# Performance work log

Measured on AMD Instinct MI355X. Metric: run time of the kernel, lower is better.

The kernel has to match this reference:

```python
import jax, jax.numpy as jnp
import numpy as np
from jax import lax

B, C, L = 64, 768, 197
DEG = 3          # KACN Chebyshev degree
KW = 3           # conv kernel size
EPS = 1e-5       # BatchNorm eps
END_X = 14.0     # RoPE grid width (14x14 patch grid + 1 CLS token)


def _conv1d(x, W):
    # x: (B, Cin, L), W: (Cout, Cin, K); padding=1 keeps length
    return lax.conv_general_dilated(x, W, window_strides=(1,), padding=[(1, 1)],
                                    dimension_numbers=('NCH', 'OIH', 'NCH'))


def _batchnorm(y, scale, bias):
    # training-mode BatchNorm1d: biased stats over (batch, length)
    mean = jnp.mean(y, axis=(0, 2), keepdims=True)
    var = jnp.var(y, axis=(0, 2), keepdims=True)
    return (y - mean) * lax.rsqrt(var + EPS) * scale[None, :, None] + bias[None, :, None]


def _kacn_proj(x, W, scale, bias):
    # KACNConv1DLayer (groups=1): cos(arange(deg+1) * arccos(tanh(x))) basis, conv, BN
    b, c, l = x.shape
    z = jnp.arccos(jnp.tanh(x))[:, :, None, :] * jnp.arange(DEG + 1, dtype=x.dtype)[None, None, :, None]
    z = jnp.cos(z).reshape(b, c * (DEG + 1), l)  # (B, C*(DEG+1), L), channel-major pairing
    return _batchnorm(_conv1d(z, W), scale, bias)


def _rope(t, cosang, sinang):
    # rotate consecutive channel pairs; t: (B, N, C), cos/sin: (N, C//2)
    b, n, c = t.shape
    p = t.reshape(b, n, c // 2, 2)
    a, bb = p[..., 0], p[..., 1]
    ra = a * cosang[None] - bb * sinang[None]
    rb = a * sinang[None] + bb * cosang[None]
    return jnp.stack([ra, rb], axis=-1).reshape(b, n, c)


def reference(x, Wq, Wk, Wv, bnq_s, bnq_b, bnk_s, bnk_b, bnv_s, bnv_b, gamma, freqs, norm_s, norm_b):
    q = _kacn_proj(x, Wq, bnq_s, bnq_b)
    k = _kacn_proj(x, Wk, bnk_s, bnk_b)
    v = _kacn_proj(x, Wv, bnv_s, bnv_b)
    b, c, l = v.shape
    Q = q.transpose(0, 2, 1)  # (B, L, C)
    K = k.transpose(0, 2, 1)
    # mixed 2D RoPE angles (num_heads=1): t_x, t_y over 14x14 grid
    t = jnp.arange(l - 1, dtype=x.dtype)
    tx = jnp.mod(t, END_X)
    ty = jnp.floor(t / END_X)
    ang = tx[:, None] * freqs[0][None, :] + ty[:, None] * freqs[1][None, :]  # (L-1, C//2)
    cosang, sinang = jnp.cos(ang), jnp.sin(ang)
    # token 0 (CLS) is not rotated
    Qr = jnp.concatenate([Q[:, :1], _rope(Q[:, 1:], cosang, sinang)], axis=1)
    Kr = jnp.concatenate([K[:, :1], _rope(K[:, 1:], cosang, sinang)], axis=1)
    energy = jnp.einsum('bic,bjc->bij', Qr, Kr)          # unscaled, as in the module
    att = jax.nn.softmax(energy, axis=-1)
    out = jnp.einsum('bcj,bij->bci', v, att)             # v @ att^T
    return _batchnorm(gamma[0] * x + out, norm_s, norm_b)


def setup_inputs() -> dict:
    key = jax.random.key(0)
    ks = jax.random.split(key, 5)
    std = 1.0 / (C * (DEG + 1) * KW)
    x = jax.random.normal(ks[0], (B, C, L), dtype=jnp.float32)
    Wq = jax.random.normal(ks[1], (C, C * (DEG + 1), KW), dtype=jnp.float32) * std
    Wk = jax.random.normal(ks[2], (C, C * (DEG + 1), KW), dtype=jnp.float32) * std
    Wv = jax.random.normal(ks[3], (C, C * (DEG + 1), KW), dtype=jnp.float32) * std
    ones = jnp.ones((C,), jnp.float32)
    zeros = jnp.zeros((C,), jnp.float32)
    # init_2d_freqs(dim=C, num_heads=1, theta=10, rotate=True).view(2, -1)
    mag = 1.0 / 10.0 ** (np.arange(0, C, 4)[: C // 4].astype(np.float32) / C)
    ang = float(jax.random.uniform(ks[4], ())) * 2.0 * np.pi
    fx = np.concatenate([mag * np.cos(ang), mag * np.cos(np.pi / 2 + ang)])
    fy = np.concatenate([mag * np.sin(ang), mag * np.sin(np.pi / 2 + ang)])
    freqs = jnp.asarray(np.stack([fx, fy], axis=0), dtype=jnp.float32)  # (2, C//2)
    return {"x": x, "Wq": Wq, "Wk": Wk, "Wv": Wv,
            "bnq_s": ones, "bnq_b": zeros, "bnk_s": ones, "bnk_b": zeros,
            "bnv_s": ones, "bnv_b": zeros,
            "gamma": jnp.zeros((1,), jnp.float32), "freqs": freqs,
            "norm_s": ones, "norm_b": zeros}
```

## Files before the change

kernel.cpp:

```cpp
#include <hip/hip_runtime.h>

#define CCH 768
#define LL  197
#define L199 199
#define KC  2304
#define KTOT 6912
#define MK2 1769472
#define NVALID 12736
#define NROW 12608

typedef __bf16 bf16x8 __attribute__((ext_vector_type(8)));
typedef float f32x4 __attribute__((ext_vector_type(4)));
typedef float f32x16 __attribute__((ext_vector_type(16)));

__device__ __forceinline__ unsigned short f2bf(float f) {
  unsigned int u = __float_as_uint(f);
  u += 0x7FFFu + ((u >> 16) & 1u);
  return (unsigned short)(u >> 16);
}
__device__ __forceinline__ float bf2f(unsigned short h) {
  return __uint_as_float(((unsigned int)h) << 16);
}

__global__ void bias_k(const float* __restrict__ Wq, const float* __restrict__ Wk,
                       const float* __restrict__ Wv, float* __restrict__ bias3) {
  int u = blockIdx.x * 256 + threadIdx.x;
  if (u >= 9 * 768) return;
  int proj = u / 2304, rem = u % 2304, tap = rem / 768, m = rem % 768;
  const float* W = proj == 0 ? Wq : (proj == 1 ? Wk : Wv);
  float s = 0.f;
  for (int c = 0; c < 768; ++c) s += W[((size_t)m * 3072 + c * 4) * 3 + tap];
  bias3[u] = s;
}

__global__ void pack_w3(const float* __restrict__ Wq, const float* __restrict__ Wk,
                        const float* __restrict__ Wv, unsigned short* __restrict__ Apack,
                        size_t pack1_halves) {
  int u = blockIdx.x * 256 + threadIdx.x;
  if (u >= MK2) return;
  int proj = blockIdx.y;
  const float* W = proj == 0 ? Wq : (proj == 1 ? Wk : Wv);
  unsigned short* Ahi = Apack + (size_t)proj * pack1_halves;
  unsigned short* Alo = Ahi + (size_t)768 * KTOT;
  int m = u / KC, kc = u % KC;
  int c = kc / 3, dm1 = kc % 3;
  int ci = c * 4 + dm1 + 1;
  const float* src = W + ((size_t)m * 3072 + ci) * 3;
#pragma unroll
  for (int tap = 0; tap < 3; ++tap) {
    float f = src[tap];
    unsigned short hi = f2bf(f);
    unsigned short lo = f2bf(f - bf2f(hi));
    size_t idx = (size_t)m * KTOT + tap * KC + kc;
    Ahi[idx] = hi;
    Alo[idx] = lo;
  }
}

__global__ void z_kernel(const float* __restrict__ x, unsigned short* __restrict__ Zhi,
                         unsigned short* __restrict__ Zlo) {
  __shared__ float zs[3][32][33];
  int c0 = blockIdx.x * 32, l0 = blockIdx.y * 32, b = blockIdx.z;
  int t = threadIdx.x;
#pragma unroll
  for (int s = 0; s < 4; ++s) {
    int u = t + 256 * s;
    int rc = u >> 5, cl = u & 31;
    float v = 0.f;
    if (l0 + cl < LL) v = x[((size_t)b * CCH + c0 + rc) * LL + l0 + cl];
    float t1 = tanhf(v);
    zs[0][rc][cl] = t1;
    zs[1][rc][cl] = 2.f * t1 * t1 - 1.f;
    zs[2][rc][cl] = t1 * (4.f * t1 * t1 - 3.f);
  }
  __syncthreads();
#pragma unroll
  for (int s = 0; s < 12; ++s) {
    int w = t + 256 * s;
    int rl = w / 96, cc = w % 96;
    if (l0 + rl < LL) {
      int cl2 = cc / 3, dm1 = cc % 3;
      float v = zs[dm1][cl2][rl];
      unsigned short hi = f2bf(v);
      unsigned short lo = f2bf(v - bf2f(hi));
      size_t row = (size_t)b * L199 + 1 + l0 + rl;
      Zhi[row * KC + c0 * 3 + cc] = hi;
      Zlo[row * KC + c0 * 3 + cc] = lo;
    }
  }
}

__global__ void zero_zpad(unsigned short* __restrict__ Zhi, unsigned short* __restrict__ Zlo) {
  int u = blockIdx.x * 256 + threadIdx.x;
  if (u >= 132 * KC) return;
  int rowi = u / KC, c = u % KC;
  size_t r = (rowi < 128) ? ((size_t)(rowi >> 1) * L199 + (size_t)(rowi & 1) * 198)
                          : ((size_t)NVALID + rowi - 128);
  Zhi[r * KC + c] = 0;
  Zlo[r * KC + c] = 0;
}

#define GLL(SRC, DST) \
  __builtin_amdgcn_global_load_lds( \
      (const __attribute__((address_space(1))) void*)(SRC), \
      (__attribute__((address_space(3))) void*)(DST), 16, 0, 0)

__global__ __launch_bounds__(512, 2) void conv_gemm3(const unsigned short* __restrict__ Apack,
                                                     const unsigned short* __restrict__ Zhi,
                                                     const unsigned short* __restrict__ Zlo,
                                                     const float* __restrict__ bias3,
                                                     float* __restrict__ Oqk,
                                                     float* __restrict__ Ov) {
  __shared__ unsigned short lds[2 * 4 * 8192];
  const int bid = blockIdx.x;
  const int xcd = bid & 7, loc = bid >> 3;
  const int wg = (xcd < 2) ? (xcd * 57 + loc) : (114 + (xcd - 2) * 56 + loc);
  const int n_t = wg / 9, rem = wg % 9;
  const int proj = rem / 3, m_t = rem % 3;
  const int m_blk = m_t * 256, n_blk = n_t * 256;
  const unsigned short* Ahi = Apack + (size_t)proj * 2 * 768 * KTOT;
  const unsigned short* Alo = Ahi + (size_t)768 * KTOT;
  const float* bias3p = bias3 + proj * 2304;
  float* Op = (proj == 2) ? Ov : Oqk + (size_t)proj * NROW * CCH;

  const int t = threadIdx.x;
  const int wave = t >> 6, lane = t & 63;
  const int wm = (wave >> 2) * 128, wn = (wave & 3) * 64;
  f32x16 acc[4][2] = {};

  const int lt = ((lane >> 4) & 1) * 512 + (lane >> 5) * 128 + (lane & 15) * 8;
  const int auoff = (wm >> 4) * 512 + lt;
  const int buoff = (wn >> 4) * 512 + lt;

  const int prow = lane & 15;
  const int kch = lane >> 4;
  const unsigned short* srcs[8];
  int doff[8];
#pragma unroll
  for (int j = 0; j < 8; ++j) {
    int u = (wave << 3) + j;
    int tile = u >> 4, p = u & 15;
    doff[j] = tile * 8192 + p * 512;
    int r;
    const unsigned short* g;
    int rs;
    if (tile < 2) {
      r = m_blk + p * 16 + prow;
      g = (tile == 0) ? Ahi : Alo;
      rs = KTOT;
    } else {
      r = n_blk + p * 16 + prow;
      if (r > 12737) r = 12737;
      g = (tile == 2) ? Zhi : Zlo;
      rs = KC;
    }
    srcs[j] = g + (size_t)r * rs + kch * 8;
  }

#pragma unroll
  for (int j = 0; j < 8; ++j) GLL(srcs[j], lds + doff[j]);
#pragma unroll
  for (int j = 0; j < 8; ++j) GLL(srcs[j] + 32, lds + 32768 + doff[j]);
#pragma unroll
  for (int j = 0; j < 8; ++j) srcs[j] += 64;

#define STEP32(LB)                                                                \
  {                                                                               \
    _Pragma("unroll") for (int ks = 0; ks < 2; ++ks) {                            \
      bf16x8 ah[4], al[4], bh[2], bl[2];                                          \
      _Pragma("unroll") for (int mb = 0; mb < 4; ++mb) {                          \
        ah[mb] = *(const bf16x8*)((LB) + auoff + mb * 1024 + ks * 256);           \
        al[mb] = *(const bf16x8*)((LB) + 8192 + auoff + mb * 1024 + ks * 256);    \
      }                                                                           \
      _Pragma("unroll") for (int nb = 0; nb < 2; ++nb) {                          \
        bh[nb] = *(const bf16x8*)((LB) + 16384 + buoff + nb * 1024 + ks * 256);   \
        bl[nb] = *(const bf16x8*)((LB) + 24576 + buoff + nb * 1024 + ks * 256);   \
      }                                                                           \
      __builtin_amdgcn_s_setprio(1);                                              \
      _Pragma("unroll") for (int mb = 0; mb < 4; ++mb)                            \
      _Pragma("unroll") for (int nb = 0; nb < 2; ++nb) {                          \
        acc[mb][nb] = __builtin_amdgcn_mfma_f32_32x32x16_bf16(ah[mb], bh[nb], acc[mb][nb], 0, 0, 0); \
        acc[mb][nb] = __builtin_amdgcn_mfma_f32_32x32x16_bf16(ah[mb], bl[nb], acc[mb][nb], 0, 0, 0); \
        acc[mb][nb] = __builtin_amdgcn_mfma_f32_32x32x16_bf16(al[mb], bh[nb], acc[mb][nb], 0, 0, 0); \
      }                                                                           \
      __builtin_amdgcn_s_setprio(0);                                              \
    }                                                                             \
  }

  const int NIT = KTOT / 32;
  for (int i = 0; i < NIT - 1; ++i) {
    asm volatile("s_waitcnt vmcnt(8)\n\ts_barrier" ::: "memory");
    __builtin_amdgcn_sched_barrier(0);
    const unsigned short* lb = lds + ((i & 1) ? 32768 : 0);
    STEP32(lb);
    asm volatile("s_waitcnt lgkmcnt(0)\n\ts_barrier" ::: "memory");
    __builtin_amdgcn_sched_barrier(0);
    if (i < NIT - 2) {
      unsigned short* ld = lds + ((i & 1) ? 32768 : 0);
#pragma unroll
      for (int j = 0; j < 8; ++j) {
        GLL(srcs[j], ld + doff[j]);
        srcs[j] += 32;
      }
    }
  }
  asm volatile("s_waitcnt vmcnt(0)\n\ts_barrier" ::: "memory");
  __builtin_amdgcn_sched_barrier(0);
  STEP32(lds + 32768);

  int rowarr[2];
  bool val[2], v0[2], v2[2];
#pragma unroll
  for (int nb = 0; nb < 2; ++nb) {
    int n = n_blk + wn + nb * 32 + (lane & 31);
    int b = n / L199, nl = n - b * L199;
    val[nb] = (n < NVALID) && (nl < LL);
    rowarr[nb] = b * LL + nl;
    v0[nb] = (nl == 0);
    v2[nb] = (nl == 196);
  }
#pragma unroll
  for (int mb = 0; mb < 4; ++mb) {
#pragma unroll
    for (int q = 0; q < 4; ++q) {
      int m = m_blk + wm + mb * 32 + q * 8 + (lane >> 5) * 4;
      f32x4 b0 = *(const f32x4*)(bias3p + m);
      f32x4 b1 = *(const f32x4*)(bias3p + 768 + m);
      f32x4 b2 = *(const f32x4*)(bias3p + 1536 + m);
      f32x4 bs = b0 + b1 + b2;
#pragma unroll
      for (int nb = 0; nb < 2; ++nb) {
        if (val[nb]) {
          f32x4 r;
          r[0] = acc[mb][nb][q * 4 + 0];
          r[1] = acc[mb][nb][q * 4 + 1];
          r[2] = acc[mb][nb][q * 4 + 2];
          r[3] = acc[mb][nb][q * 4 + 3];
          r += bs;
          if (v0[nb]) r -= b0;
          if (v2[nb]) r -= b2;
          *(f32x4*)(Op + (size_t)rowarr[nb] * CCH + m) = r;
        }
      }
    }
  }
#undef STEP32
}

__global__ void zero_f32(float* __restrict__ p, int n) {
  int u = blockIdx.x * 256 + threadIdx.x;
  if (u < n) p[u] = 0.f;
}

__global__ void bn_stats(const float* __restrict__ Oqk, const float* __restrict__ Ov,
                         float* __restrict__ Ssum, float* __restrict__ Ssq) {
  int proj = blockIdx.z;
  int cb = blockIdx.x * 64;
  int rb = blockIdx.y;
  int t = threadIdx.x;
  int ch = cb + (t & 63);
  int phase = t >> 6;
  const float* Op = (proj == 2) ? Ov : Oqk + (size_t)proj * NROW * CCH;
  float s = 0.f, q = 0.f;
  for (int r = rb * 394 + phase; r < rb * 394 + 394; r += 4) {
    float v = Op[(size_t)r * CCH + ch];
    s += v; q += v * v;
  }
  __shared__ float rs[256], rq[256];
  rs[t] = s; rq[t] = q;
  __syncthreads();
  if (t < 64) {
    float S = rs[t] + rs[t + 64] + rs[t + 128] + rs[t + 192];
    float Q = rq[t] + rq[t + 64] + rq[t + 128] + rq[t + 192];
    atomicAdd(&Ssum[proj * CCH + cb + t], S);
    atomicAdd(&Ssq[proj * CCH + cb + t], Q);
  }
}

__global__ void bn_fin(const float* __restrict__ Ssum, const float* __restrict__ Ssq,
                       const float* __restrict__ sq, const float* __restrict__ bq,
                       const float* __restrict__ sk, const float* __restrict__ bk,
                       const float* __restrict__ sv, const float* __restrict__ bv,
                       float* __restrict__ abn) {
  int u = blockIdx.x * 256 + threadIdx.x;
  if (u >= 3 * CCH) return;
  int proj = u / CCH, ch = u % CCH;
  float mean = Ssum[u] / 12608.f;
  float var = Ssq[u] / 12608.f - mean * mean;
  const float* sc = proj == 0 ? sq : (proj == 1 ? sk : sv);
  const float* bi = proj == 0 ? bq : (proj == 1 ? bk : bv);
  float a = sc[ch] * rsqrtf(var + 1e-5f);
  abn[u * 2] = a;
  abn[u * 2 + 1] = bi[ch] - mean * a;
}

__global__ void rope_pack(const float* __restrict__ Oqk, const float* __restrict__ abn,
                          const float* __restrict__ freqs, float* __restrict__ Qr,
                          float* __restrict__ Kr) {
  size_t u = (size_t)blockIdx.x * 256 + threadIdx.x;
  if (u >= 64ull * LL * 384) return;
  int c2 = (int)(u % 384);
  int l = (int)((u / 384) % LL);
  int b = (int)(u / (384ull * LL));
  size_t rowO = ((size_t)b * LL + l) * CCH + 2 * c2;
  const float* Ok = Oqk + (size_t)NROW * CCH;
  float q0 = Oqk[rowO], q1 = Oqk[rowO + 1];
  float k0 = Ok[rowO], k1 = Ok[rowO + 1];
  float aq0 = abn[(2 * c2) * 2],                bq0 = abn[(2 * c2) * 2 + 1];
  float aq1 = abn[(2 * c2 + 1) * 2],            bq1 = abn[(2 * c2 + 1) * 2 + 1];
  float ak0 = abn[(CCH + 2 * c2) * 2],          bk0 = abn[(CCH + 2 * c2) * 2 + 1];
  float ak1 = abn[(CCH + 2 * c2 + 1) * 2],      bk1 = abn[(CCH + 2 * c2 + 1) * 2 + 1];
  q0 = q0 * aq0 + bq0; q1 = q1 * aq1 + bq1;
  k0 = k0 * ak0 + bk0; k1 = k1 * ak1 + bk1;
  if (l > 0) {
    int tt = l - 1;
    float tx = (float)(tt % 14), ty = (float)(tt / 14);
    float ang = tx * freqs[c2] + ty * freqs[384 + c2];
    float sn, cs;
    sincosf(ang, &sn, &cs);
    float r0 = q0 * cs - q1 * sn, r1 = q0 * sn + q1 * cs;
    q0 = r0; q1 = r1;
    r0 = k0 * cs - k1 * sn; r1 = k0 * sn + k1 * cs;
    k0 = r0; k1 = r1;
  }
  size_t rowT = ((size_t)b * LL + l) * CCH + 2 * c2;
  Qr[rowT] = q0; Qr[rowT + 1] = q1;
  Kr[rowT] = k0; Kr[rowT + 1] = k1;
}

__global__ void energy_k(const float* __restrict__ Qr, const float* __restrict__ Kr,
                         float* __restrict__ E) {
  __shared__ float Qs[32][33], Ks[32][33];
  int i0 = blockIdx.x * 32, j0 = blockIdx.y * 32, b = blockIdx.z;
  int t = threadIdx.x, tj = t & 31, ti = t >> 5;
  float acc[4] = {0.f, 0.f, 0.f, 0.f};
  const float* Qb = Qr + (size_t)b * LL * CCH;
  const float* Kb = Kr + (size_t)b * LL * CCH;
  for (int k0 = 0; k0 < CCH; k0 += 32) {
    __syncthreads();
#pragma unroll
    for (int s = 0; s < 4; ++s) {
      int u = t + 256 * s, r = u >> 5, cc = u & 31;
      Qs[r][cc] = (i0 + r < LL) ? Qb[(size_t)(i0 + r) * CCH + k0 + cc] : 0.f;
      Ks[r][cc] = (j0 + r < LL) ? Kb[(size_t)(j0 + r) * CCH + k0 + cc] : 0.f;
    }
    __syncthreads();
#pragma unroll
    for (int kk = 0; kk < 32; ++kk) {
      float kv = Ks[tj][kk];
#pragma unroll
      for (int q = 0; q < 4; ++q) acc[q] += Qs[ti * 4 + q][kk] * kv;
    }
  }
#pragma unroll
  for (int q = 0; q < 4; ++q) {
    int i = i0 + ti * 4 + q, j = j0 + tj;
    if (i < LL && j < LL) E[((size_t)b * LL + i) * LL + j] = acc[q];
  }
}

__global__ void softmax_k(float* __restrict__ E) {
  int row = blockIdx.x;
  int lane = threadIdx.x;
  float* Er = E + (size_t)row * LL;
  float v[4];
  float m = -3.4e38f;
#pragma unroll
  for (int q = 0; q < 4; ++q) {
    int j = lane + 64 * q;
    v[q] = (j < LL) ? Er[j] : -3.4e38f;
    m = fmaxf(m, v[q]);
  }
  for (int off = 32; off; off >>= 1) m = fmaxf(m, __shfl_down(m, off));
  m = __shfl(m, 0);
  float s = 0.f;
#pragma unroll
  for (int q = 0; q < 4; ++q) {
    int j = lane + 64 * q;
    v[q] = (j < LL) ? expf(v[q] - m) : 0.f;
    s += v[q];
  }
  for (int off = 32; off; off >>= 1) s += __shfl_down(s, off);
  s = __shfl(s, 0);
  float inv = 1.f / s;
#pragma unroll
  for (int q = 0; q < 4; ++q) {
    int j = lane + 64 * q;
    if (j < LL) Er[j] = v[q] * inv;
  }
}

__global__ void av_k(const float* __restrict__ att, const float* __restrict__ Ov,
                     const float* __restrict__ abn, float* __restrict__ OA) {
  __shared__ float As[32][33];
  __shared__ float Vs[32][64];
  int i0 = blockIdx.x * 32, c0 = blockIdx.y * 64, b = blockIdx.z;
  int t = threadIdx.x, tc = t & 63, tq = t >> 6;
  const float* attb = att + (size_t)b * LL * LL;
  float acc[8] = {};
  for (int j0 = 0; j0 < LL; j0 += 32) {
    __syncthreads();
#pragma unroll
    for (int s = 0; s < 4; ++s) {
      int u = t + 256 * s, r = u >> 5, cc = u & 31;
      As[r][cc] = (i0 + r < LL && j0 + cc < LL) ? attb[(size_t)(i0 + r) * LL + j0 + cc] : 0.f;
    }
#pragma unroll
    for (int s = 0; s < 8; ++s) {
      int u = t + 256 * s, r = u >> 6, cc = u & 63;
      Vs[r][cc] = (j0 + r < LL) ? Ov[((size_t)b * LL + j0 + r) * CCH + c0 + cc] : 0.f;
    }
    __syncthreads();
#pragma unroll
    for (int jj = 0; jj < 32; ++jj) {
      float vv = Vs[jj][tc];
#pragma unroll
      for (int q = 0; q < 8; ++q) acc[q] += As[tq * 8 + q][jj] * vv;
    }
  }
  float a = abn[(2 * CCH + c0 + tc) * 2], bb = abn[(2 * CCH + c0 + tc) * 2 + 1];
#pragma unroll
  for (int q = 0; q < 8; ++q) {
    int i = i0 + tq * 8 + q;
    if (i < LL) OA[((size_t)b * LL + i) * CCH + c0 + tc] = a * acc[q] + bb;
  }
}

__global__ void trans_y(const float* __restrict__ OA, const float* __restrict__ x,
                        const float* __restrict__ gamma, float* __restrict__ Y) {
  __shared__ float Ts[32][33];
  int l0 = blockIdx.x * 32, c0 = blockIdx.y * 32, b = blockIdx.z;
  int t = threadIdx.x;
  float g = gamma[0];
#pragma unroll
  for (int s = 0; s < 4; ++s) {
    int u = t + 256 * s, r = u >> 5, cc = u & 31;
    Ts[r][cc] = (l0 + r < LL) ? OA[((size_t)b * LL + l0 + r) * CCH + c0 + cc] : 0.f;
  }
  __syncthreads();
#pragma unroll
  for (int s = 0; s < 4; ++s) {
    int u = t + 256 * s, rc = u >> 5, cl = u & 31;
    if (l0 + cl < LL) {
      size_t idx = ((size_t)b * CCH + c0 + rc) * LL + l0 + cl;
      Y[idx] = g * x[idx] + Ts[cl][rc];
    }
  }
}

__global__ void bn_y(const float* __restrict__ Y, const float* __restrict__ ns,
                     const float* __restrict__ nb, float* __restrict__ fab) {
  int c = blockIdx.x;
  int t = threadIdx.x;
  float s = 0.f, q = 0.f;
  for (int u = t; u < 12608; u += 256) {
    int b = u / LL, l = u % LL;
    float v = Y[((size_t)b * CCH + c) * LL + l];
    s += v; q += v * v;
  }
  __shared__ float rs[256], rq[256];
  rs[t] = s; rq[t] = q;
  __syncthreads();
  for (int off = 128; off; off >>= 1) {
    if (t < off) { rs[t] += rs[t + off]; rq[t] += rq[t + off]; }
    __syncthreads();
  }
  if (t == 0) {
    float mean = rs[0] / 12608.f, var = rq[0] / 12608.f - mean * mean;
    float a = ns[c] * rsqrtf(var + 1e-5f);
    fab[c * 2] = a;
    fab[c * 2 + 1] = nb[c] - mean * a;
  }
}

__global__ void final_k(const float* __restrict__ Y, const float* __restrict__ fab,
                        float* __restrict__ out) {
  size_t u = (size_t)blockIdx.x * 256 + threadIdx.x;
  if (u >= 64ull * CCH * LL) return;
  int c = (int)((u / LL) % CCH);
  out[u] = fab[c * 2] * Y[u] + fab[c * 2 + 1];
}

extern "C" void kernel_launch(void* const* d_in, const int* in_sizes, int n_in,
                              void* d_out, int out_size, void* d_ws, size_t ws_size,
                              hipStream_t stream) {
  const float* x = (const float*)d_in[0];
  const float* Wq = (const float*)d_in[1];
  const float* Wk = (const float*)d_in[2];
  const float* Wv = (const float*)d_in[3];
  const float* bnq_s = (const float*)d_in[4];
  const float* bnq_b = (const float*)d_in[5];
  const float* bnk_s = (const float*)d_in[6];
  const float* bnk_b = (const float*)d_in[7];
  const float* bnv_s = (const float*)d_in[8];
  const float* bnv_b = (const float*)d_in[9];
  const float* gamma = (const float*)d_in[10];
  const float* freqs = (const float*)d_in[11];
  const float* norm_s = (const float*)d_in[12];
  const float* norm_b = (const float*)d_in[13];
  float* out = (float*)d_out;

  char* ws = (char*)d_ws;
  const size_t QRSZ  = 38731776;
  const size_t PACK1 = 21233664;
  const size_t ZSZ   = 58705920;

  const size_t OFS_PACK = 0;
  const size_t OFS_Z    = 3 * PACK1;
  const size_t OFS_ZLO  = OFS_Z + ZSZ;
  const size_t OFS_O    = OFS_ZLO + ZSZ;
  const size_t OFS_MISC = OFS_O + 2 * QRSZ;

  unsigned short* Apack = (unsigned short*)(ws + OFS_PACK);
  unsigned short* Zhi = (unsigned short*)(ws + OFS_Z);
  unsigned short* Zlo = (unsigned short*)(ws + OFS_ZLO);
  float* Oqk = (float*)(ws + OFS_O);
  float* bias3 = (float*)(ws + OFS_MISC);
  float* Ssum = (float*)(ws + OFS_MISC + 27648);
  float* Ssq  = (float*)(ws + OFS_MISC + 36864);
  float* abn  = (float*)(ws + OFS_MISC + 46080);
  float* fab  = (float*)(ws + OFS_MISC + 64512);
  float* Ov = out;
  float* Qr = (float*)(ws + OFS_Z);
  float* Kr = (float*)(ws + OFS_Z + QRSZ);
  float* E  = (float*)(ws + OFS_Z + 2 * QRSZ);
  float* OA = (float*)(ws + OFS_Z);
  float* Y  = (float*)(ws + OFS_Z + QRSZ);

  bias_k<<<dim3(27), 256, 0, stream>>>(Wq, Wk, Wv, bias3);
  zero_zpad<<<dim3((132 * KC + 255) / 256), 256, 0, stream>>>(Zhi, Zlo);
  z_kernel<<<dim3(24, 7, 64), 256, 0, stream>>>(x, Zhi, Zlo);
  pack_w3<<<dim3((MK2 + 255) / 256, 3), 256, 0, stream>>>(Wq, Wk, Wv, Apack, PACK1 / 2);
  conv_gemm3<<<dim3(450), 512, 0, stream>>>(Apack, Zhi, Zlo, bias3, Oqk, Ov);

  zero_f32<<<dim3(18), 256, 0, stream>>>(Ssum, 4608);
  bn_stats<<<dim3(12, 32, 3), 256, 0, stream>>>(Oqk, Ov, Ssum, Ssq);
  bn_fin<<<dim3(9), 256, 0, stream>>>(Ssum, Ssq, bnq_s, bnq_b, bnk_s, bnk_b, bnv_s, bnv_b, abn);
  rope_pack<<<dim3((unsigned)((64ull * LL * 384 + 255) / 256)), 256, 0, stream>>>(Oqk, abn, freqs, Qr, Kr);
  energy_k<<<dim3(7, 7, 64), 256, 0, stream>>>(Qr, Kr, E);
  softmax_k<<<dim3(64 * LL), 64, 0, stream>>>(E);
  av_k<<<dim3(7, 12, 64), 256, 0, stream>>>(E, Ov, abn, OA);
  trans_y<<<dim3(7, 24, 64), 256, 0, stream>>>(OA, x, gamma, Y);
  bn_y<<<dim3(CCH), 256, 0, stream>>>(Y, norm_s, norm_b, fab);
  final_k<<<dim3((unsigned)((64ull * CCH * LL + 255) / 256)), 256, 0, stream>>>(Y, fab, out);
}
```

Baseline: 2.272 ms.

## Interleave GEMM global-to-LDS loads with MFMA phases in fine-grained pipeline

Restructures the split-bf16 GEMM main loop from a coarse two-stage double buffer into four per-M-block phases per K step. Each phase loads A fragments, issues two global-to-LDS loads for a later stage, and runs its MFMAs, with barriers between phases. This spreads memory traffic across compute and staggers loads across buffers so the copy latency is hidden better. In exchange it adds many more barriers per iteration and relies on subtle buffer and vmcnt accounting that could race or stall.

```diff
diff --git a/kernel.cpp b/kernel.cpp
--- a/kernel.cpp
+++ b/kernel.cpp
@@ -157,56 +157,94 @@
     srcs[j] = g + (size_t)r * rs + kch * 8;
   }
 
+  const int NIT = KTOT / 32;
 #pragma unroll
   for (int j = 0; j < 8; ++j) GLL(srcs[j], lds + doff[j]);
 #pragma unroll
-  for (int j = 0; j < 8; ++j) GLL(srcs[j] + 32, lds + 32768 + doff[j]);
-#pragma unroll
-  for (int j = 0; j < 8; ++j) srcs[j] += 64;
-
-#define STEP32(LB)                                                                \
-  {                                                                               \
-    _Pragma("unroll") for (int ks = 0; ks < 2; ++ks) {                            \
-      bf16x8 ah[4], al[4], bh[2], bl[2];                                          \
-      _Pragma("unroll") for (int mb = 0; mb < 4; ++mb) {                          \
-        ah[mb] = *(const bf16x8*)((LB) + auoff + mb * 1024 + ks * 256);           \
-        al[mb] = *(const bf16x8*)((LB) + 8192 + auoff + mb * 1024 + ks * 256);    \
+  for (int j = 0; j < 6; ++j) GLL(srcs[j] + 32, lds + 32768 + doff[j]);
+  asm volatile("s_waitcnt vmcnt(6)\n\ts_barrier" ::: "memory");
+  __builtin_amdgcn_sched_barrier(0);
+
+  for (int i = 0; i < NIT; ++i) {
+    const unsigned short* lb = lds + ((i & 1) ? 32768 : 0);
+    unsigned short* othbuf = lds + ((i & 1) ? 0 : 32768);
+    unsigned short* curbuf = lds + ((i & 1) ? 32768 : 0);
+    const int koff_prev = 32 * (i + 1);
+    const int koff_cur  = 32 * (i + 2);
+    const bool stage_prev = (i < NIT - 1);
+    const bool stage_cur  = (i < NIT - 2);
+
+    bf16x8 bh[2][2], bl[2][2];
+    bf16x8 ah[2], al[2];
+
+#pragma unroll
+    for (int ks = 0; ks < 2; ++ks) {
+#pragma unroll
+      for (int nb = 0; nb < 2; ++nb) {
+        bh[nb][ks] = *(const bf16x8*)(lb + 16384 + buoff + nb * 1024 + ks * 256);
+        bl[nb][ks] = *(const bf16x8*)(lb + 24576 + buoff + nb * 1024 + ks * 256);
+      }
+      ah[ks] = *(const bf16x8*)(lb + auoff + ks * 256);
+      al[ks] = *(const bf16x8*)(lb + 8192 + auoff + ks * 256);
+    }
+    if (stage_prev) {
+      GLL(srcs[6] + koff_prev, othbuf + doff[6]);
+      GLL(srcs[7] + koff_prev, othbuf + doff[7]);
+    }
+    asm volatile("s_barrier\n\ts_waitcnt lgkmcnt(0)" ::: "memory");
+    __builtin_amdgcn_sched_barrier(0);
+    __builtin_amdgcn_s_setprio(1);
+#pragma unroll
+    for (int p = 0; p < 3; ++p)
+#pragma unroll
+      for (int ks = 0; ks < 2; ++ks)
+#pragma unroll
+        for (int nb = 0; nb < 2; ++nb) {
+          acc[0][nb] = __builtin_amdgcn_mfma_f32_32x32x16_bf16(
+              p == 2 ? al[ks] : ah[ks], p == 1 ? bl[nb][ks] : bh[nb][ks], acc[0][nb], 0, 0, 0);
+        }
+    __builtin_amdgcn_s_setprio(0);
+    asm volatile("s_barrier" ::: "memory");
+    __builtin_amdgcn_sched_barrier(0);
+
+#define PHASEQ(Q)                                                                 \
+    {                                                                             \
+      _Pragma("unroll") for (int ks = 0; ks < 2; ++ks) {                          \
+        ah[ks] = *(const bf16x8*)(lb + auoff + (Q) * 1024 + ks * 256);            \
+        al[ks] = *(const bf16x8*)(lb + 8192 + auoff + (Q) * 1024 + ks * 256);     \
       }                                                                           \
+      if (stage_cur) {                                                            \
+        GLL(srcs[2 * ((Q) - 1)] + koff_cur, curbuf + doff[2 * ((Q) - 1)]);        \
+        GLL(srcs[2 * ((Q) - 1) + 1] + koff_cur, curbuf + doff[2 * ((Q) - 1) + 1]);\
+      }                                                                           \
+      asm volatile("s_barrier\n\ts_waitcnt lgkmcnt(0)" ::: "memory");             \
+      __builtin_amdgcn_sched_barrier(0);                                          \
+      __builtin_amdgcn_s_setprio(1);                                              \
+      _Pragma("unroll") for (int p = 0; p < 3; ++p)                               \
+      _Pragma("unroll") for (int ks = 0; ks < 2; ++ks)                            \
       _Pragma("unroll") for (int nb = 0; nb < 2; ++nb) {                          \
-        bh[nb] = *(const bf16x8*)((LB) + 16384 + buoff + nb * 1024 + ks * 256);   \
-        bl[nb] = *(const bf16x8*)((LB) + 24576 + buoff + nb * 1024 + ks * 256);   \
-      }                                                                           \
-      __builtin_amdgcn_s_setprio(1);                                              \
-      _Pragma("unroll") for (int mb = 0; mb < 4; ++mb)                            \
-      _Pragma("unroll") for (int nb = 0; nb < 2; ++nb) {                          \
-        acc[mb][nb] = __builtin_amdgcn_mfma_f32_32x32x16_bf16(ah[mb], bh[nb], acc[mb][nb], 0, 0, 0); \
-        acc[mb][nb] = __builtin_amdgcn_mfma_f32_32x32x16_bf16(ah[mb], bl[nb], acc[mb][nb], 0, 0, 0); \
-        acc[mb][nb] = __builtin_amdgcn_mfma_f32_32x32x16_bf16(al[mb], bh[nb], acc[mb][nb], 0, 0, 0); \
+        acc[Q][nb] = __builtin_amdgcn_mfma_f32_32x32x16_bf16(                     \
+            p == 2 ? al[ks] : ah[ks], p == 1 ? bl[nb][ks] : bh[nb][ks],           \
+            acc[Q][nb], 0, 0, 0);                                                 \
       }                                                                           \
       __builtin_amdgcn_s_setprio(0);                                              \
-    }                                                                             \
-  }
-
-  const int NIT = KTOT / 32;
-  for (int i = 0; i < NIT - 1; ++i) {
-    asm volatile("s_waitcnt vmcnt(8)\n\ts_barrier" ::: "memory");
+    }
+
+    PHASEQ(1)
+    asm volatile("s_barrier" ::: "memory");
     __builtin_amdgcn_sched_barrier(0);
-    const unsigned short* lb = lds + ((i & 1) ? 32768 : 0);
-    STEP32(lb);
-    asm volatile("s_waitcnt lgkmcnt(0)\n\ts_barrier" ::: "memory");
+    PHASEQ(2)
+    asm volatile("s_barrier" ::: "memory");
     __builtin_amdgcn_sched_barrier(0);
+    PHASEQ(3)
     if (i < NIT - 2) {
-      unsigned short* ld = lds + ((i & 1) ? 32768 : 0);
-#pragma unroll
-      for (int j = 0; j < 8; ++j) {
-        GLL(srcs[j], ld + doff[j]);
-        srcs[j] += 32;
-      }
-    }
-  }
-  asm volatile("s_waitcnt vmcnt(0)\n\ts_barrier" ::: "memory");
-  __builtin_amdgcn_sched_barrier(0);
-  STEP32(lds + 32768);
+      asm volatile("s_waitcnt vmcnt(6)\n\ts_barrier" ::: "memory");
+    } else if (i == NIT - 2) {
+      asm volatile("s_waitcnt vmcnt(0)\n\ts_barrier" ::: "memory");
+    }
+    __builtin_amdgcn_sched_barrier(0);
+#undef PHASEQ
+  }
 
   int rowarr[2];
   bool val[2], v0[2], v2[2];
@@ -244,7 +282,6 @@
       }
     }
   }
-#undef STEP32
 }
 
 __global__ void zero_f32(float* __restrict__ p, int n) {
```

New measurement: 2.031 ms. 1.12x faster.

## Restructure conv GEMM prefetch pipeline and parallelize bias reduction across wavefronts

Applied to the files above, without the earlier changes.

The bias reduction kernel now assigns one 64-lane wavefront per output and reduces with shuffles, instead of one thread looping over 768 strided elements. This removes a long serial tail from a 27-block launch. The conv GEMM main loop is reorganized: each iteration first issues the global-to-LDS loads for the next K chunk into the other buffer, then runs two per-ks phases. Each phase loads the fragments, syncs, and issues the MFMAs grouped by hi/lo pass. This adds extra barriers per iteration and changes how much loads overlap with compute, and it relies on the buffer-reuse ordering being correct.

```diff
diff --git a/kernel.cpp b/kernel.cpp
--- a/kernel.cpp
+++ b/kernel.cpp
@@ -24,13 +24,15 @@
 
 __global__ void bias_k(const float* __restrict__ Wq, const float* __restrict__ Wk,
                        const float* __restrict__ Wv, float* __restrict__ bias3) {
-  int u = blockIdx.x * 256 + threadIdx.x;
-  if (u >= 9 * 768) return;
-  int proj = u / 2304, rem = u % 2304, tap = rem / 768, m = rem % 768;
+  int w = (blockIdx.x * 256 + threadIdx.x) >> 6;
+  int lane = threadIdx.x & 63;
+  if (w >= 9 * 768) return;
+  int proj = w / 2304, rem = w % 2304, tap = rem / 768, m = rem % 768;
   const float* W = proj == 0 ? Wq : (proj == 1 ? Wk : Wv);
   float s = 0.f;
-  for (int c = 0; c < 768; ++c) s += W[((size_t)m * 3072 + c * 4) * 3 + tap];
-  bias3[u] = s;
+  for (int c = lane; c < 768; c += 64) s += W[((size_t)m * 3072 + c * 4) * 3 + tap];
+  for (int off = 32; off; off >>= 1) s += __shfl_down(s, off);
+  if (lane == 0) bias3[w] = s;
 }
 
 __global__ void pack_w3(const float* __restrict__ Wq, const float* __restrict__ Wk,
@@ -157,56 +159,52 @@
     srcs[j] = g + (size_t)r * rs + kch * 8;
   }
 
+  const int NIT = KTOT / 32;
 #pragma unroll
   for (int j = 0; j < 8; ++j) GLL(srcs[j], lds + doff[j]);
-#pragma unroll
-  for (int j = 0; j < 8; ++j) GLL(srcs[j] + 32, lds + 32768 + doff[j]);
-#pragma unroll
-  for (int j = 0; j < 8; ++j) srcs[j] += 64;
-
-#define STEP32(LB)                                                                \
+
+#define PHASE_KS(KS)                                                              \
   {                                                                               \
-    _Pragma("unroll") for (int ks = 0; ks < 2; ++ks) {                            \
-      bf16x8 ah[4], al[4], bh[2], bl[2];                                          \
-      _Pragma("unroll") for (int mb = 0; mb < 4; ++mb) {                          \
-        ah[mb] = *(const bf16x8*)((LB) + auoff + mb * 1024 + ks * 256);           \
-        al[mb] = *(const bf16x8*)((LB) + 8192 + auoff + mb * 1024 + ks * 256);    \
-      }                                                                           \
-      _Pragma("unroll") for (int nb = 0; nb < 2; ++nb) {                          \
-        bh[nb] = *(const bf16x8*)((LB) + 16384 + buoff + nb * 1024 + ks * 256);   \
-        bl[nb] = *(const bf16x8*)((LB) + 24576 + buoff + nb * 1024 + ks * 256);   \
-      }                                                                           \
-      __builtin_amdgcn_s_setprio(1);                                              \
-      _Pragma("unroll") for (int mb = 0; mb < 4; ++mb)                            \
-      _Pragma("unroll") for (int nb = 0; nb < 2; ++nb) {                          \
-        acc[mb][nb] = __builtin_amdgcn_mfma_f32_32x32x16_bf16(ah[mb], bh[nb], acc[mb][nb], 0, 0, 0); \
-        acc[mb][nb] = __builtin_amdgcn_mfma_f32_32x32x16_bf16(ah[mb], bl[nb], acc[mb][nb], 0, 0, 0); \
-        acc[mb][nb] = __builtin_amdgcn_mfma_f32_32x32x16_bf16(al[mb], bh[nb], acc[mb][nb], 0, 0, 0); \
-      }                                                                           \
-      __builtin_amdgcn_s_setprio(0);                                              \
+    bf16x8 ah[4], al[4], bh[2], bl[2];                                            \
+    _Pragma("unroll") for (int mb = 0; mb < 4; ++mb) {                            \
+      ah[mb] = *(const bf16x8*)(lb + auoff + mb * 1024 + (KS) * 256);             \
+      al[mb] = *(const bf16x8*)(lb + 8192 + auoff + mb * 1024 + (KS) * 256);      \
     }                                                                             \
-  }
-
-  const int NIT = KTOT / 32;
-  for (int i = 0; i < NIT - 1; ++i) {
-    asm volatile("s_waitcnt vmcnt(8)\n\ts_barrier" ::: "memory");
+    _Pragma("unroll") for (int nb = 0; nb < 2; ++nb) {                            \
+      bh[nb] = *(const bf16x8*)(lb + 16384 + buoff + nb * 1024 + (KS) * 256);     \
+      bl[nb] = *(const bf16x8*)(lb + 24576 + buoff + nb * 1024 + (KS) * 256);     \
+    }                                                                             \
+    asm volatile("s_barrier\n\ts_waitcnt lgkmcnt(0)" ::: "memory");               \
+    __builtin_amdgcn_sched_barrier(0);                                            \
+    __builtin_amdgcn_s_setprio(1);                                                \
+    _Pragma("unroll") for (int p = 0; p < 3; ++p)                                 \
+    _Pragma("unroll") for (int mb = 0; mb < 4; ++mb)                              \
+    _Pragma("unroll") for (int nb = 0; nb < 2; ++nb) {                            \
+      acc[mb][nb] = __builtin_amdgcn_mfma_f32_32x32x16_bf16(                      \
+          p == 2 ? al[mb] : ah[mb], p == 1 ? bl[nb] : bh[nb], acc[mb][nb],        \
+          0, 0, 0);                                                               \
+    }                                                                             \
+    __builtin_amdgcn_s_setprio(0);                                                \
+  }
+
+  for (int i = 0; i < NIT; ++i) {
+    const unsigned short* lb = lds + ((i & 1) ? 32768 : 0);
+    unsigned short* nxt = lds + ((i & 1) ? 0 : 32768);
+    asm volatile("s_barrier" ::: "memory");
     __builtin_amdgcn_sched_barrier(0);
-    const unsigned short* lb = lds + ((i & 1) ? 32768 : 0);
-    STEP32(lb);
-    asm volatile("s_waitcnt lgkmcnt(0)\n\ts_barrier" ::: "memory");
+    if (i + 1 < NIT) {
+      const int ko = 32 * (i + 1);
+#pragma unroll
+      for (int j = 0; j < 8; ++j) GLL(srcs[j] + ko, nxt + doff[j]);
+      asm volatile("s_waitcnt vmcnt(8)\n\ts_barrier" ::: "memory");
+    } else {
+      asm volatile("s_waitcnt vmcnt(0)\n\ts_barrier" ::: "memory");
+    }
     __builtin_amdgcn_sched_barrier(0);
-    if (i < NIT - 2) {
-      unsigned short* ld = lds + ((i & 1) ? 32768 : 0);
-#pragma unroll
-      for (int j = 0; j < 8; ++j) {
-        GLL(srcs[j], ld + doff[j]);
-        srcs[j] += 32;
-      }
-    }
-  }
-  asm volatile("s_waitcnt vmcnt(0)\n\ts_barrier" ::: "memory");
-  __builtin_amdgcn_sched_barrier(0);
-  STEP32(lds + 32768);
+    PHASE_KS(0)
+    PHASE_KS(1)
+  }
+#undef PHASE_KS
 
   int rowarr[2];
   bool val[2], v0[2], v2[2];
@@ -244,7 +242,6 @@
       }
     }
   }
-#undef STEP32
 }
 
 __global__ void zero_f32(float* __restrict__ p, int n) {
@@ -527,7 +524,7 @@
   float* OA = (float*)(ws + OFS_Z);
   float* Y  = (float*)(ws + OFS_Z + QRSZ);
 
-  bias_k<<<dim3(27), 256, 0, stream>>>(Wq, Wk, Wv, bias3);
+  bias_k<<<dim3(1728), 256, 0, stream>>>(Wq, Wk, Wv, bias3);
   zero_zpad<<<dim3((132 * KC + 255) / 256), 256, 0, stream>>>(Zhi, Zlo);
   z_kernel<<<dim3(24, 7, 64), 256, 0, stream>>>(x, Zhi, Zlo);
   pack_w3<<<dim3((MK2 + 255) / 256, 3), 256, 0, stream>>>(Wq, Wk, Wv, Apack, PACK1 / 2);
```

Result: faster. 2.079 ms (-8.5%).
